# Kernel optimization log

Hardware: AMD Instinct MI355X
Metric: run time of the kernel (lower is better)

## Reference

```python
import jax, jax.numpy as jnp
import numpy as np
from jax import lax

B, N, S, K = 16, 8192, 1024, 32
FACTOR = 1.0
EPS_BN = 1e-5


def farthest_point_sample(xyz, npoint):
    # xyz: [B, N, 3] -> idx [B, npoint]. Deterministic start at index 0
    # (torch version starts at a random index; start choice doesn't change the math pattern).
    b, n, _ = xyz.shape
    bidx = jnp.arange(b)

    def step(carry, _):
        distance, farthest = carry
        centroid = xyz[bidx, farthest]                      # [B, 3]
        dist = jnp.sum((xyz - centroid[:, None, :]) ** 2, -1)  # [B, N]
        distance = jnp.minimum(distance, dist)
        new_far = jnp.argmax(distance, axis=-1)
        return (distance, new_far), farthest

    init = (jnp.full((b, n), 1e10, xyz.dtype), jnp.zeros((b,), jnp.int32))
    _, idxs = lax.scan(step, init, None, length=npoint)
    return idxs.T  # [B, npoint]


def square_distance(src, dst):
    # [B,Ns,3] x [B,Nd,3] -> [B,Ns,Nd]
    d = -2.0 * jnp.einsum('bnc,bmc->bnm', src, dst)
    d += jnp.sum(src ** 2, -1)[:, :, None]
    d += jnp.sum(dst ** 2, -1)[:, None, :]
    return d


def safe_cdist(x):
    # x: [B, C, S]; pairwise euclidean over rows -> [B, C, C]; zero-safe sqrt
    diff = x[:, :, None, :] - x[:, None, :, :]          # [B, C, C, S]
    sq = jnp.sum(diff * diff, -1)
    pos = sq > 0
    return jnp.where(pos, jnp.sqrt(jnp.where(pos, sq, 1.0)), 0.0)


def batchnorm(x, gamma, beta, axes):
    mean = jnp.mean(x, axes, keepdims=True)
    var = jnp.var(x, axes, keepdims=True)  # biased, as in torch BN normalization
    return (x - mean) / jnp.sqrt(var + EPS_BN) * gamma + beta


def reference(xyz, bn1_gamma, bn1_beta, bn2_gamma, bn2_beta):
    b = xyz.shape[0]
    # --- FPS sampling ---
    fps_idx = farthest_point_sample(lax.stop_gradient(xyz), S)          # [B,S]
    new_xyz = jnp.take_along_axis(xyz, fps_idx[:, :, None], axis=1)     # [B,S,3]
    # --- kNN grouping ---
    sq = square_distance(lax.stop_gradient(new_xyz), lax.stop_gradient(xyz))  # [B,S,N]
    _, knn_idx = lax.top_k(-sq, K)                                      # [B,S,K] indices
    grouped = jax.vmap(lambda p, i: p[i])(xyz, knn_idx)                 # [B,S,K,3]
    diff = grouped - new_xyz[:, :, None, :]
    std = jnp.std(diff, ddof=1)                                         # scalar, unbiased like torch.std
    knn_norm = diff / (std + 1e-5)
    center = jnp.broadcast_to(new_xyz[:, :, None, :], (b, S, K, 3))
    knn_xyz = jnp.concatenate([knn_norm, center], axis=-1)              # [B,S,K,6]
    # --- Pooling over neighbors ---
    x = jnp.transpose(knn_xyz, (0, 3, 1, 2))                            # [B,6,S,K]
    lc = jnp.max(x, -1) + jnp.mean(x, -1)                               # [B,6,S]
    lc = jax.nn.relu(batchnorm(lc, bn1_gamma[None, :, None], bn1_beta[None, :, None], (0, 2)))
    # --- Consecutive representation (cdist + superdiagonal factor) ---
    tfcw = safe_cdist(lc)                                               # [B,6,6]
    i = jnp.arange(5)
    tfcw = tfcw.at[:, i, i + 1].multiply(FACTOR)
    # --- Pooling2 ---
    feat = tfcw.reshape(b, -1)                                          # [B,36]
    feat = jax.nn.relu(batchnorm(feat, bn2_gamma[None, :], bn2_beta[None, :], (0,)))
    return feat


def setup_inputs() -> dict:
    key = jax.random.key(0)
    k1, = jax.random.split(key, 1)
    return {
        'xyz': jax.random.normal(k1, (B, N, 3), dtype=jnp.float32),
        'bn1_gamma': jnp.ones((6,), jnp.float32),
        'bn1_beta': jnp.zeros((6,), jnp.float32),
        'bn2_gamma': jnp.ones((36,), jnp.float32),
        'bn2_beta': jnp.zeros((36,), jnp.float32),
    }
```

## Files before the change

kernel.cpp:

```cpp
#include <hip/hip_runtime.h>
#include <hip/hip_bf16.h>

constexpr int BB = 16;
constexpr int NN = 8192;
constexpr int SS = 1024;
constexpr int KK = 32;
constexpr int BUFC = 256;

__device__ __forceinline__ float b2f(__hip_bfloat16 h) { return __bfloat162float(h); }

__device__ __forceinline__ unsigned mkey32(float d) {
    unsigned u = __float_as_uint(d);
    return u ^ (0x80000000u | (unsigned)((int)u >> 31));
}

__device__ __forceinline__ unsigned long long dist_key(const float* __restrict__ pb,
                                                       int idx, float qx, float qy,
                                                       float qz, float qq) {
    float px = pb[idx * 3 + 0];
    float py = pb[idx * 3 + 1];
    float pz = pb[idx * 3 + 2];
    float dot = __fadd_rn(__fadd_rn(__fmul_rn(qx, px), __fmul_rn(qy, py)), __fmul_rn(qz, pz));
    float pp  = __fadd_rn(__fadd_rn(__fmul_rn(px, px), __fmul_rn(py, py)), __fmul_rn(pz, pz));
    float d = __fadd_rn(__fadd_rn(__fmul_rn(-2.0f, dot), qq), pp);
    return ((unsigned long long)mkey32(d) << 32) | (unsigned)idx;
}

template <int CTRL, int RMASK>
__device__ __forceinline__ unsigned long long dppmove_u64(unsigned long long v) {
    int lo = (int)(unsigned)v, hi = (int)(unsigned)(v >> 32);
    int nlo = __builtin_amdgcn_update_dpp(lo, lo, CTRL, RMASK, 0xf, false);
    int nhi = __builtin_amdgcn_update_dpp(hi, hi, CTRL, RMASK, 0xf, false);
    return ((unsigned long long)(unsigned)nhi << 32) | (unsigned)nlo;
}

template <int CTRL, int RMASK>
__device__ __forceinline__ double dppmax_f64(double v) {
    double m = __longlong_as_double(
        dppmove_u64<CTRL, RMASK>((unsigned long long)__double_as_longlong(v)));
    return fmax(v, m);
}

__device__ __forceinline__ double wave_max_dpp_f64(double v) {
    v = dppmax_f64<0x121, 0xf>(v);
    v = dppmax_f64<0x122, 0xf>(v);
    v = dppmax_f64<0x124, 0xf>(v);
    v = dppmax_f64<0x128, 0xf>(v);
    v = dppmax_f64<0x142, 0xa>(v);
    v = dppmax_f64<0x143, 0xc>(v);
    return v;
}

__device__ __forceinline__ unsigned long long bitonic64(unsigned long long v, int lane) {
#pragma unroll
    for (int k = 2; k <= 64; k <<= 1) {
#pragma unroll
        for (int j = k >> 1; j > 0; j >>= 1) {
            unsigned long long p = __shfl_xor(v, j);
            bool up = ((lane & k) == 0);
            bool lower = ((lane & j) == 0);
            bool take_min = (up == lower);
            v = take_min ? (p < v ? p : v) : (p > v ? p : v);
        }
    }
    return v;
}

__device__ __forceinline__ unsigned expand3(unsigned v) {
    v &= 0x3FFu;
    v = (v | (v << 16)) & 0x030000FFu;
    v = (v | (v << 8))  & 0x0300F00Fu;
    v = (v | (v << 4))  & 0x030C30C3u;
    v = (v | (v << 2))  & 0x09249249u;
    return v;
}

__global__ __launch_bounds__(256) void convert_kernel(
    const void* __restrict__ xyz_raw, const void* __restrict__ g1r,
    const void* __restrict__ b1r, const void* __restrict__ g2r,
    const void* __restrict__ b2r, float* __restrict__ xyzf,
    float* __restrict__ params, void* __restrict__ out_raw) {
    const unsigned short* u = (const unsigned short*)xyz_raw;
    unsigned short s = u[2 * (threadIdx.x & 63)];
    int e = (s >> 7) & 0xFF;
    unsigned long long m = __ballot(e >= 100 && e <= 140);
    bool isbf = __popcll(m) > 48;

    const int NT = BB * NN * 3;
    int tid = blockIdx.x * blockDim.x + threadIdx.x;
    int stride = gridDim.x * blockDim.x;
    if (isbf) {
        const __hip_bfloat16* p = (const __hip_bfloat16*)xyz_raw;
        for (int i = tid; i < NT; i += stride) xyzf[i] = b2f(p[i]);
    } else {
        const float* p = (const float*)xyz_raw;
        for (int i = tid; i < NT; i += stride) xyzf[i] = p[i];
    }
    if (blockIdx.x == 0 && threadIdx.x < 85) {
        int t = threadIdx.x;
        if (t == 84) {
            params[84] = isbf ? 1.0f : 0.0f;
        } else {
            const void* src; int off;
            if (t < 6)       { src = g1r; off = t; }
            else if (t < 12) { src = b1r; off = t - 6; }
            else if (t < 48) { src = g2r; off = t - 12; }
            else             { src = b2r; off = t - 48; }
            params[t] = isbf ? b2f(((const __hip_bfloat16*)src)[off])
                             : ((const float*)src)[off];
        }
    }
    if (blockIdx.x == 1 && threadIdx.x < 64) {
        for (int i = threadIdx.x; i < 576; i += 64) {
            if (isbf) ((__hip_bfloat16*)out_raw)[i] = __float2bfloat16(1.0f);
            else      ((float*)out_raw)[i] = 1.0f;
        }
    }
}

__global__ __attribute__((amdgpu_flat_work_group_size(512, 512)))
__attribute__((amdgpu_waves_per_eu(2, 2)))
void fps_kernel(const float* __restrict__ xyzf, float* __restrict__ new_xyz) {
    constexpr int T = 512, P = NN / T;
    const int b = blockIdx.x, t = threadIdx.x;
    const float* xb = xyzf + (size_t)b * NN * 3;

    __shared__ float sxyz[NN * 3];
    __shared__ unsigned sortk[NN];
    __shared__ double skey[2][8];
    __shared__ float sred[6][8];
    __shared__ float sbb[6];

    for (int i = t; i < NN * 3; i += T) sxyz[i] = xb[i];
    __syncthreads();

    {
        float mn[3] = {3.4e38f, 3.4e38f, 3.4e38f};
        float mx[3] = {-3.4e38f, -3.4e38f, -3.4e38f};
        for (int j = 0; j < P; j++) {
            int p = t + j * T;
#pragma unroll
            for (int c = 0; c < 3; c++) {
                float v = sxyz[p * 3 + c];
                mn[c] = fminf(mn[c], v);
                mx[c] = fmaxf(mx[c], v);
            }
        }
#pragma unroll
        for (int o = 32; o > 0; o >>= 1) {
#pragma unroll
            for (int c = 0; c < 3; c++) {
                mn[c] = fminf(mn[c], __shfl_xor(mn[c], o));
                mx[c] = fmaxf(mx[c], __shfl_xor(mx[c], o));
            }
        }
        int wv = t >> 6, ln = t & 63;
        if (ln == 0) {
#pragma unroll
            for (int c = 0; c < 3; c++) { sred[c][wv] = mn[c]; sred[3 + c][wv] = mx[c]; }
        }
        __syncthreads();
        if (t < 6) {
            bool ismin = t < 3;
            float v = sred[t][0];
            for (int w = 1; w < 8; w++) v = ismin ? fminf(v, sred[t][w]) : fmaxf(v, sred[t][w]);
            sbb[t] = v;
        }
        __syncthreads();
    }

    {
        float bx = sbb[0], by = sbb[1], bz = sbb[2];
        float qsx = 63.0f / fmaxf(sbb[3] - bx, 1e-9f);
        float qsy = 63.0f / fmaxf(sbb[4] - by, 1e-9f);
        float qsz = 63.0f / fmaxf(sbb[5] - bz, 1e-9f);
        for (int p = t; p < NN; p += T) {
            unsigned qx = (unsigned)min(63, (int)((sxyz[p * 3 + 0] - bx) * qsx));
            unsigned qy = (unsigned)min(63, (int)((sxyz[p * 3 + 1] - by) * qsy));
            unsigned qz = (unsigned)min(63, (int)((sxyz[p * 3 + 2] - bz) * qsz));
            unsigned m = (expand3(qx) << 2) | (expand3(qy) << 1) | expand3(qz);
            sortk[p] = (m << 13) | (unsigned)p;
        }
        __syncthreads();
        for (unsigned k = 2; k <= (unsigned)NN; k <<= 1) {
            for (unsigned j = k >> 1; j > 0; j >>= 1) {
#pragma unroll
                for (int r = 0; r < NN / 2 / T; r++) {
                    unsigned gid = (unsigned)(r * T + t);
                    unsigned i = ((gid & ~(j - 1)) << 1) | (gid & (j - 1));
                    unsigned p2 = i | j;
                    unsigned a = sortk[i], c2 = sortk[p2];
                    bool up = ((i & k) == 0);
                    if ((a > c2) == up) { sortk[i] = c2; sortk[p2] = a; }
                }
                __syncthreads();
            }
        }
    }

    float px[P], py[P], pz[P], ds[P];
    int nidx[P];
    float lox = 3.4e38f, loy = 3.4e38f, loz = 3.4e38f;
    float hix = -3.4e38f, hiy = -3.4e38f, hiz = -3.4e38f;
#pragma unroll
    for (int j = 0; j < P; j++) {
        unsigned oi = sortk[t * P + j] & 8191u;
        float x = sxyz[oi * 3 + 0];
        float y = sxyz[oi * 3 + 1];
        float z = sxyz[oi * 3 + 2];
        px[j] = x; py[j] = y; pz[j] = z;
        ds[j] = 1e10f;
        nidx[j] = (int)~oi;
        lox = fminf(lox, x); hix = fmaxf(hix, x);
        loy = fminf(loy, y); hiy = fmaxf(hiy, y);
        loz = fminf(loz, z); hiz = fmaxf(hiz, z);
    }

    float cx = xb[0], cy = xb[1], cz = xb[2];
    if (t == 0) {
        float* o = new_xyz + (size_t)b * SS * 3;
        o[0] = cx; o[1] = cy; o[2] = cz;
    }
    const int wave = t >> 6, lane = t & 63;

    double bk = 0.0;
    float tb = 1e10f;

    for (int step = 1; step < SS; step++) {
        float ax = fmaxf(fmaxf(__fsub_rn(lox, cx), __fsub_rn(cx, hix)), 0.0f);
        float ay = fmaxf(fmaxf(__fsub_rn(loy, cy), __fsub_rn(cy, hiy)), 0.0f);
        float az = fmaxf(fmaxf(__fsub_rn(loz, cz), __fsub_rn(cz, hiz)), 0.0f);
        float lbd = ax * ax + ay * ay + az * az;
        if (lbd * 0.999f < tb) {
            double nbk = 0.0;
#pragma unroll
            for (int j = 0; j < P; j++) {
                float dx = __fsub_rn(px[j], cx);
                float dy = __fsub_rn(py[j], cy);
                float dz = __fsub_rn(pz[j], cz);
                float d = __fadd_rn(__fadd_rn(__fmul_rn(dx, dx), __fmul_rn(dy, dy)),
                                    __fmul_rn(dz, dz));
                float mm = fminf(ds[j], d);
                ds[j] = mm;
                double kk = __hiloint2double(__float_as_int(mm), nidx[j]);
                nbk = fmax(nbk, kk);
            }
            bk = nbk;
            tb = __uint_as_float((unsigned)__double2hiint(bk));
        }

        double wk = wave_max_dpp_f64(bk);
        const int par = step & 1;
        if (lane == 63) skey[par][wave] = wk;
        __syncthreads();

        double k0 = fmax(skey[par][0], skey[par][1]);
        double k1 = fmax(skey[par][2], skey[par][3]);
        double k2 = fmax(skey[par][4], skey[par][5]);
        double k3 = fmax(skey[par][6], skey[par][7]);
        double bkk = fmax(fmax(k0, k1), fmax(k2, k3));

        unsigned gidx = ~(unsigned)(unsigned long long)__double_as_longlong(bkk);
        cx = sxyz[gidx * 3 + 0];
        cy = sxyz[gidx * 3 + 1];
        cz = sxyz[gidx * 3 + 2];
        if (t == 0) {
            float* o = new_xyz + ((size_t)b * SS + step) * 3;
            o[0] = cx; o[1] = cy; o[2] = cz;
        }
    }
}

__global__ __launch_bounds__(256, 2) void knn_kernel(const float* __restrict__ xyzf,
                                                     const float* __restrict__ new_xyz,
                                                     float* __restrict__ A,
                                                     double* __restrict__ qstats) {
    __shared__ unsigned long long buf[4][BUFC];
    const int t = threadIdx.x;
    const int lane = t & 63, wv = t >> 6;
    const int w = blockIdx.x * 4 + wv;
    const int b = w >> 10, s = w & 1023;

    const float* q = new_xyz + ((size_t)b * SS + s) * 3;
    float qx = q[0], qy = q[1], qz = q[2];
    float qq = __fadd_rn(__fadd_rn(__fmul_rn(qx, qx), __fmul_rn(qy, qy)), __fmul_rn(qz, qz));

    const float* pb = xyzf + (size_t)b * NN * 3;
    const unsigned long long ltmask = (1ull << lane) - 1ull;

    unsigned long long lmin = ~0ull;
    for (int j = 0; j < 128; j++) {
        unsigned long long key = dist_key(pb, j * 64 + lane, qx, qy, qz, qq);
        lmin = key < lmin ? key : lmin;
    }

    unsigned long long vs = bitonic64(lmin, lane);
    unsigned long long That = __shfl(vs, 31);

    for (int i = lane; i < BUFC; i += 64) buf[wv][i] = ~0ull;
    int base = 0;
    for (int j = 0; j < 128; j++) {
        unsigned long long key = dist_key(pb, j * 64 + lane, qx, qy, qz, qq);
        bool f = key <= That;
        unsigned long long bal = __ballot(f);
        int pos = base + __popcll(bal & ltmask);
        if (f && pos < BUFC) buf[wv][pos] = key;
        base += __popcll(bal);
    }

    if (base > BUFC) {
        unsigned lo = 0, hi = (unsigned)(That >> 32);
        for (int it = 0; it < 32; it++) {
            unsigned mid = lo + ((hi - lo) >> 1);
            int c = 0;
            for (int j = 0; j < 128; j++) {
                unsigned long long key = dist_key(pb, j * 64 + lane, qx, qy, qz, qq);
                c += ((unsigned)(key >> 32) <= mid) ? 1 : 0;
            }
#pragma unroll
            for (int o = 32; o > 0; o >>= 1) c += __shfl_xor(c, o);
            if (c >= 32) hi = mid; else lo = mid + 1;
        }
        That = ((unsigned long long)hi << 32) | 0xFFFFFFFFull;
        for (int i = lane; i < BUFC; i += 64) buf[wv][i] = ~0ull;
        base = 0;
        for (int j = 0; j < 128; j++) {
            unsigned long long key = dist_key(pb, j * 64 + lane, qx, qy, qz, qq);
            bool f = key <= That;
            unsigned long long bal = __ballot(f);
            int pos = base + __popcll(bal & ltmask);
            if (f && pos < BUFC) buf[wv][pos] = key;
            base += __popcll(bal);
        }
        if (base > BUFC) base = BUFC;
    }

    int M = base;
    unsigned long long kept = ~0ull;
    if (M <= 64) {
        unsigned long long v = (lane < M) ? buf[wv][lane] : ~0ull;
        v = bitonic64(v, lane);
        kept = v;
    } else {
        unsigned long long c0 = buf[wv][lane];
        unsigned long long c1 = buf[wv][64 + lane];
        unsigned long long c2 = buf[wv][128 + lane];
        unsigned long long c3 = buf[wv][192 + lane];
        for (int r = 0; r < KK; r++) {
            unsigned long long m01 = c0 < c1 ? c0 : c1;
            unsigned long long m23 = c2 < c3 ? c2 : c3;
            unsigned long long mm = m01 < m23 ? m01 : m23;
#pragma unroll
            for (int o = 32; o > 0; o >>= 1) {
                unsigned long long t2 = __shfl_xor(mm, o);
                mm = t2 < mm ? t2 : mm;
            }
            if (lane == r) kept = mm;
            c0 = (c0 == mm) ? ~0ull : c0;
            c1 = (c1 == mm) ? ~0ull : c1;
            c2 = (c2 == mm) ? ~0ull : c2;
            c3 = (c3 == mm) ? ~0ull : c3;
        }
    }

    bool act = (lane < KK);
    float gx = 0.0f, gy = 0.0f, gz = 0.0f;
    if (act) {
        unsigned nidx = (unsigned)kept;
        gx = pb[nidx * 3 + 0];
        gy = pb[nidx * 3 + 1];
        gz = pb[nidx * 3 + 2];
    }
    float dx = __fsub_rn(gx, qx);
    float dy = __fsub_rn(gy, qy);
    float dz = __fsub_rn(gz, qz);
    float mx = act ? dx : -3.402823466e38f;
    float my = act ? dy : -3.402823466e38f;
    float mz = act ? dz : -3.402823466e38f;
    float sx = act ? dx : 0.0f;
    float sy = act ? dy : 0.0f;
    float sz = act ? dz : 0.0f;
    double s1 = act ? ((double)dx + (double)dy + (double)dz) : 0.0;
    double s2 = act ? ((double)dx * dx + (double)dy * dy + (double)dz * dz) : 0.0;
#pragma unroll
    for (int o = 32; o > 0; o >>= 1) {
        mx = fmaxf(mx, __shfl_xor(mx, o));
        my = fmaxf(my, __shfl_xor(my, o));
        mz = fmaxf(mz, __shfl_xor(mz, o));
        sx += __shfl_xor(sx, o);
        sy += __shfl_xor(sy, o);
        sz += __shfl_xor(sz, o);
        s1 += __shfl_xor(s1, o);
        s2 += __shfl_xor(s2, o);
    }
    if (lane == 0) {
        float* a = A + ((size_t)b * SS + s) * 3;
        a[0] = __fadd_rn(mx, __fmul_rn(sx, 0.03125f));
        a[1] = __fadd_rn(my, __fmul_rn(sy, 0.03125f));
        a[2] = __fadd_rn(mz, __fmul_rn(sz, 0.03125f));
        qstats[2 * w + 0] = s1;
        qstats[2 * w + 1] = s2;
    }
}

__global__ __launch_bounds__(256) void reduce_stats_kernel(const double* __restrict__ qstats,
                                                           double* __restrict__ stats) {
    __shared__ double r1[4], r2[4];
    int t = threadIdx.x;
    double a = 0.0, bsum = 0.0;
    for (int i = t; i < BB * SS; i += 256) { a += qstats[2 * i]; bsum += qstats[2 * i + 1]; }
#pragma unroll
    for (int o = 32; o > 0; o >>= 1) { a += __shfl_xor(a, o); bsum += __shfl_xor(bsum, o); }
    int wv = t >> 6, ln = t & 63;
    if (ln == 0) { r1[wv] = a; r2[wv] = bsum; }
    __syncthreads();
    if (t == 0) {
        stats[0] = r1[0] + r1[1] + r1[2] + r1[3];
        stats[1] = r2[0] + r2[1] + r2[2] + r2[3];
    }
}

__global__ __launch_bounds__(256) void lc_kernel(const float* __restrict__ new_xyz,
                                                 const float* __restrict__ A,
                                                 const double* __restrict__ stats,
                                                 float* __restrict__ lc,
                                                 double* __restrict__ bn1acc) {
    __shared__ double red[4];
    const int b = blockIdx.x / 6, c = blockIdx.x % 6;
    const int t = threadIdx.x;
    const double n = (double)BB * SS * KK * 3;
    double sd = stats[0], sq = stats[1];
    double var = (sq - sd * sd / n) / (n - 1.0);
    float stdv = (float)sqrt(var);
    float denom = __fadd_rn(stdv, 1e-5f);

    double s1 = 0.0, s2 = 0.0;
    for (int r = 0; r < 4; r++) {
        int s = r * 256 + t;
        float v;
        if (c < 3) {
            v = A[((size_t)b * SS + s) * 3 + c] / denom;
        } else {
            float ww = new_xyz[((size_t)b * SS + s) * 3 + (c - 3)];
            v = __fadd_rn(ww, ww);
        }
        lc[((size_t)b * 6 + c) * SS + s] = v;
        s1 += (double)v;
        s2 += (double)v * (double)v;
    }
#pragma unroll
    for (int off = 32; off > 0; off >>= 1) { s1 += __shfl_down(s1, off); s2 += __shfl_down(s2, off); }
    int wv = t >> 6, ln = t & 63;
    if (ln == 0) red[wv] = s1;
    __syncthreads();
    if (t == 0) atomicAdd(&bn1acc[c * 2 + 0], red[0] + red[1] + red[2] + red[3]);
    __syncthreads();
    if (ln == 0) red[wv] = s2;
    __syncthreads();
    if (t == 0) atomicAdd(&bn1acc[c * 2 + 1], red[0] + red[1] + red[2] + red[3]);
}

__global__ __launch_bounds__(256) void cdist_kernel(const float* __restrict__ lc,
                                                    const double* __restrict__ bn1acc,
                                                    const float* __restrict__ params,
                                                    float* __restrict__ tf) {
    __shared__ float sy[6 * SS];
    const int b = blockIdx.x, t = threadIdx.x;
    float mean[6], sde[6], gg[6], bt[6];
    const double n = (double)BB * SS;
#pragma unroll
    for (int c = 0; c < 6; c++) {
        double m = bn1acc[c * 2 + 0] / n;
        double v = bn1acc[c * 2 + 1] / n - m * m;
        mean[c] = (float)m;
        sde[c] = sqrtf((float)v + 1e-5f);
        gg[c] = params[c];
        bt[c] = params[6 + c];
    }
    for (int r = 0; r < 24; r++) {
        int g = r * 256 + t;
        int c = g >> 10;
        float v = lc[(size_t)b * 6 * SS + g];
        float y = (v - mean[c]) / sde[c] * gg[c] + bt[c];
        sy[g] = fmaxf(y, 0.0f);
    }
    __syncthreads();
    if (t < 6) tf[b * 36 + t * 7] = 0.0f;

    const int w = t >> 6, lane = t & 63;
    const int PI[15] = {0,0,0,0,0,1,1,1,1,2,2,2,3,3,4};
    const int PJ[15] = {1,2,3,4,5,2,3,4,5,3,4,5,4,5,5};
    for (int r = 0; r < 4; r++) {
        int p = w + r * 4;
        if (p < 15) {
            int i = PI[p], j = PJ[p];
            float acc = 0.0f;
            for (int m2 = 0; m2 < 16; m2++) {
                int s = lane + m2 * 64;
                float d = sy[i * SS + s] - sy[j * SS + s];
                acc += d * d;
            }
#pragma unroll
            for (int off = 32; off > 0; off >>= 1) acc += __shfl_down(acc, off);
            if (lane == 0) {
                float v = acc > 0.0f ? sqrtf(acc) : 0.0f;
                const float FACTOR = 1.0f;
                tf[b * 36 + i * 6 + j] = (j == i + 1) ? v * FACTOR : v;
                tf[b * 36 + j * 6 + i] = v;
            }
        }
    }
}

__global__ __launch_bounds__(64) void bn2_kernel(const float* __restrict__ tf,
                                                 const float* __restrict__ params,
                                                 void* __restrict__ out_raw) {
    int f = threadIdx.x;
    if (f >= 36) return;
    bool isbf = params[84] != 0.0f;
    float x[16]; float sum = 0.0f;
#pragma unroll
    for (int b = 0; b < 16; b++) { x[b] = tf[b * 36 + f]; sum += x[b]; }
    float mean = sum * 0.0625f;
    float vs = 0.0f;
#pragma unroll
    for (int b = 0; b < 16; b++) { float d = x[b] - mean; vs += d * d; }
    float var = vs * 0.0625f;
    float denom = sqrtf(var + 1e-5f);
    float g = params[12 + f], bb = params[48 + f];
#pragma unroll
    for (int b = 0; b < 16; b++) {
        float y = (x[b] - mean) / denom * g + bb;
        y = fmaxf(y, 0.0f);
        if (isbf) ((__hip_bfloat16*)out_raw)[b * 36 + f] = __float2bfloat16(y);
        else      ((float*)out_raw)[b * 36 + f] = y;
    }
}

extern "C" void kernel_launch(void* const* d_in, const int* in_sizes, int n_in,
                              void* d_out, int out_size, void* d_ws, size_t ws_size,
                              hipStream_t stream) {
    const void* xyz_raw = d_in[0];
    const void* g1r = d_in[1]; const void* b1r = d_in[2];
    const void* g2r = d_in[3]; const void* b2r = d_in[4];
    {
        const void* six[2] = {nullptr, nullptr}; int n6 = 0;
        const void* t36[2] = {nullptr, nullptr}; int n36 = 0;
        const void* big = nullptr;
        for (int i = 0; i < n_in; i++) {
            if (in_sizes[i] == BB * NN * 3) big = d_in[i];
            else if (in_sizes[i] == 6  && n6  < 2) six[n6++]  = d_in[i];
            else if (in_sizes[i] == 36 && n36 < 2) t36[n36++] = d_in[i];
        }
        if (big && n6 == 2 && n36 == 2) {
            xyz_raw = big; g1r = six[0]; b1r = six[1]; g2r = t36[0]; b2r = t36[1];
        }
    }

    char* ws = (char*)d_ws;
    float* xyzf    = (float*)(ws + 0);
    float* new_xyz = (float*)(ws + 1572864);
    float* A       = (float*)(ws + 1769472);
    float* lc      = (float*)(ws + 1966080);
    float* tf      = (float*)(ws + 2359296);
    double* stats  = (double*)(ws + 2361600);
    double* bn1acc = stats + 2;
    float* params  = (float*)(ws + 2361712);
    double* qstats = (double*)(ws + 2362112);

    hipMemsetAsync(stats, 0, 14 * sizeof(double), stream);
    hipLaunchKernelGGL(convert_kernel, dim3(512), dim3(256), 0, stream,
                       xyz_raw, g1r, b1r, g2r, b2r, xyzf, params, d_out);
    hipLaunchKernelGGL(fps_kernel,          dim3(16),   dim3(512), 0, stream, xyzf, new_xyz);
    hipLaunchKernelGGL(knn_kernel,          dim3(4096), dim3(256), 0, stream, xyzf, new_xyz, A, qstats);
    hipLaunchKernelGGL(reduce_stats_kernel, dim3(1),    dim3(256), 0, stream, qstats, stats);
    hipLaunchKernelGGL(lc_kernel,           dim3(96),   dim3(256), 0, stream, new_xyz, A, stats, lc, bn1acc);
    hipLaunchKernelGGL(cdist_kernel,        dim3(16),   dim3(256), 0, stream, lc, bn1acc, params, tf);
    hipLaunchKernelGGL(bn2_kernel,          dim3(1),    dim3(64),  0, stream, tf, params, d_out);

    (void)in_sizes; (void)n_in; (void)out_size; (void)ws_size;
}
```

Before: 1.183 ms.

## Split FPS per-thread points into two culled halves and skip idle wave reductions

Each thread's 16 points are split into two halves, each with its own bounding box and cached max, so the distance update can be skipped for one half when its box lower bound cannot beat the half's current maximum. The wave-level max reduction runs only when some lane in the wave actually updated; otherwise the previous wave max is reused. The winning lane publishes its coordinates next to its key in shared memory, removing the dependent shared-memory lookup of the centroid after the barrier. This adds branches and registers, and relies on the matching lane to write the key, so ties or stale wave values must stay consistent.

```diff
diff --git a/kernel.cpp b/kernel.cpp
--- a/kernel.cpp
+++ b/kernel.cpp
@@ -73,6 +73,15 @@
     v = (v | (v << 4))  & 0x030C30C3u;
     v = (v | (v << 2))  & 0x09249249u;
     return v;
+}
+
+__device__ __forceinline__ void sel2(double& k, float& x, float& y, float& z,
+                                     double kb, float xb, float yb, float zb) {
+    bool g = kb > k;
+    k = g ? kb : k;
+    x = g ? xb : x;
+    y = g ? yb : y;
+    z = g ? zb : z;
 }
 
 __global__ __launch_bounds__(256) void convert_kernel(
@@ -128,6 +137,7 @@
     __shared__ float sxyz[NN * 3];
     __shared__ unsigned sortk[NN];
     __shared__ double skey[2][8];
+    __shared__ float4 scoord[2][8];
     __shared__ float sred[6][8];
     __shared__ float sbb[6];
 
@@ -200,8 +210,10 @@
 
     float px[P], py[P], pz[P], ds[P];
     int nidx[P];
-    float lox = 3.4e38f, loy = 3.4e38f, loz = 3.4e38f;
-    float hix = -3.4e38f, hiy = -3.4e38f, hiz = -3.4e38f;
+    float l0x = 3.4e38f, l0y = 3.4e38f, l0z = 3.4e38f;
+    float h0x = -3.4e38f, h0y = -3.4e38f, h0z = -3.4e38f;
+    float l1x = 3.4e38f, l1y = 3.4e38f, l1z = 3.4e38f;
+    float h1x = -3.4e38f, h1y = -3.4e38f, h1z = -3.4e38f;
 #pragma unroll
     for (int j = 0; j < P; j++) {
         unsigned oi = sortk[t * P + j] & 8191u;
@@ -211,10 +223,18 @@
         px[j] = x; py[j] = y; pz[j] = z;
         ds[j] = 1e10f;
         nidx[j] = (int)~oi;
-        lox = fminf(lox, x); hix = fmaxf(hix, x);
-        loy = fminf(loy, y); hiy = fmaxf(hiy, y);
-        loz = fminf(loz, z); hiz = fmaxf(hiz, z);
-    }
+        if (j < 8) {
+            l0x = fminf(l0x, x); h0x = fmaxf(h0x, x);
+            l0y = fminf(l0y, y); h0y = fmaxf(h0y, y);
+            l0z = fminf(l0z, z); h0z = fmaxf(h0z, z);
+        } else {
+            l1x = fminf(l1x, x); h1x = fmaxf(h1x, x);
+            l1y = fminf(l1y, y); h1y = fmaxf(h1y, y);
+            l1z = fminf(l1z, z); h1z = fmaxf(h1z, z);
+        }
+    }
+    const float lox = fminf(l0x, l1x), loy = fminf(l0y, l1y), loz = fminf(l0z, l1z);
+    const float hix = fmaxf(h0x, h1x), hiy = fmaxf(h0y, h1y), hiz = fmaxf(h0z, h1z);
 
     float cx = xb[0], cy = xb[1], cz = xb[2];
     if (t == 0) {
@@ -223,47 +243,98 @@
     }
     const int wave = t >> 6, lane = t & 63;
 
-    double bk = 0.0;
-    float tb = 1e10f;
+    double hk0 = 0.0, hk1 = 0.0;
+    float tb0 = 1e10f, tb1 = 1e10f;
+    unsigned wkL = 0u, wkH = 0u;
 
     for (int step = 1; step < SS; step++) {
-        float ax = fmaxf(fmaxf(__fsub_rn(lox, cx), __fsub_rn(cx, hix)), 0.0f);
-        float ay = fmaxf(fmaxf(__fsub_rn(loy, cy), __fsub_rn(cy, hiy)), 0.0f);
-        float az = fmaxf(fmaxf(__fsub_rn(loz, cz), __fsub_rn(cz, hiz)), 0.0f);
-        float lbd = ax * ax + ay * ay + az * az;
-        if (lbd * 0.999f < tb) {
-            double nbk = 0.0;
-#pragma unroll
-            for (int j = 0; j < P; j++) {
-                float dx = __fsub_rn(px[j], cx);
-                float dy = __fsub_rn(py[j], cy);
-                float dz = __fsub_rn(pz[j], cz);
-                float d = __fadd_rn(__fadd_rn(__fmul_rn(dx, dx), __fmul_rn(dy, dy)),
-                                    __fmul_rn(dz, dz));
-                float mm = fminf(ds[j], d);
-                ds[j] = mm;
-                double kk = __hiloint2double(__float_as_int(mm), nidx[j]);
-                nbk = fmax(nbk, kk);
-            }
-            bk = nbk;
-            tb = __uint_as_float((unsigned)__double2hiint(bk));
-        }
-
-        double wk = wave_max_dpp_f64(bk);
+        float ax = fmaxf(fmaxf(lox - cx, cx - hix), 0.0f);
+        float ay = fmaxf(fmaxf(loy - cy, cy - hiy), 0.0f);
+        float az = fmaxf(fmaxf(loz - cz, cz - hiz), 0.0f);
+        float lbdO = ax * ax + ay * ay + az * az;
+        bool did = false;
+        if (lbdO * 0.999f < fmaxf(tb0, tb1)) {
+            float a0x = fmaxf(fmaxf(l0x - cx, cx - h0x), 0.0f);
+            float a0y = fmaxf(fmaxf(l0y - cy, cy - h0y), 0.0f);
+            float a0z = fmaxf(fmaxf(l0z - cz, cz - h0z), 0.0f);
+            float lbd0 = a0x * a0x + a0y * a0y + a0z * a0z;
+            if (lbd0 * 0.999f < tb0) {
+                double kk[8];
+#pragma unroll
+                for (int j = 0; j < 8; j++) {
+                    float dx = __fsub_rn(px[j], cx);
+                    float dy = __fsub_rn(py[j], cy);
+                    float dz = __fsub_rn(pz[j], cz);
+                    float d = __fadd_rn(__fadd_rn(__fmul_rn(dx, dx), __fmul_rn(dy, dy)),
+                                        __fmul_rn(dz, dz));
+                    float mm = fminf(ds[j], d);
+                    ds[j] = mm;
+                    kk[j] = __hiloint2double(__float_as_int(mm), nidx[j]);
+                }
+                double m0 = fmax(kk[0], kk[1]), m1 = fmax(kk[2], kk[3]);
+                double m2 = fmax(kk[4], kk[5]), m3 = fmax(kk[6], kk[7]);
+                hk0 = fmax(fmax(m0, m1), fmax(m2, m3));
+                tb0 = __uint_as_float((unsigned)__double2hiint(hk0));
+                did = true;
+            }
+            float a1x = fmaxf(fmaxf(l1x - cx, cx - h1x), 0.0f);
+            float a1y = fmaxf(fmaxf(l1y - cy, cy - h1y), 0.0f);
+            float a1z = fmaxf(fmaxf(l1z - cz, cz - h1z), 0.0f);
+            float lbd1 = a1x * a1x + a1y * a1y + a1z * a1z;
+            if (lbd1 * 0.999f < tb1) {
+                double kk[8];
+#pragma unroll
+                for (int j = 0; j < 8; j++) {
+                    float dx = __fsub_rn(px[8 + j], cx);
+                    float dy = __fsub_rn(py[8 + j], cy);
+                    float dz = __fsub_rn(pz[8 + j], cz);
+                    float d = __fadd_rn(__fadd_rn(__fmul_rn(dx, dx), __fmul_rn(dy, dy)),
+                                        __fmul_rn(dz, dz));
+                    float mm = fminf(ds[8 + j], d);
+                    ds[8 + j] = mm;
+                    kk[j] = __hiloint2double(__float_as_int(mm), nidx[8 + j]);
+                }
+                double m0 = fmax(kk[0], kk[1]), m1 = fmax(kk[2], kk[3]);
+                double m2 = fmax(kk[4], kk[5]), m3 = fmax(kk[6], kk[7]);
+                hk1 = fmax(fmax(m0, m1), fmax(m2, m3));
+                tb1 = __uint_as_float((unsigned)__double2hiint(hk1));
+                did = true;
+            }
+        }
+        double bk = fmax(hk0, hk1);
+        unsigned long long bkb = (unsigned long long)__double_as_longlong(bk);
+
+        unsigned myi = ~(unsigned)bkb;
+        float gx = sxyz[myi * 3 + 0];
+        float gy = sxyz[myi * 3 + 1];
+        float gz = sxyz[myi * 3 + 2];
+
+        if (__ballot(did) != 0ull) {
+            double wkv = wave_max_dpp_f64(bk);
+            unsigned long long wb = (unsigned long long)__double_as_longlong(wkv);
+            wkL = (unsigned)__builtin_amdgcn_readlane((int)(unsigned)wb, 63);
+            wkH = (unsigned)__builtin_amdgcn_readlane((int)(unsigned)(wb >> 32), 63);
+        }
+        unsigned long long wkb = ((unsigned long long)wkH << 32) | wkL;
         const int par = step & 1;
-        if (lane == 63) skey[par][wave] = wk;
+        if (bkb == wkb) {
+            skey[par][wave] = bk;
+            scoord[par][wave] = make_float4(gx, gy, gz, 0.0f);
+        }
         __syncthreads();
 
-        double k0 = fmax(skey[par][0], skey[par][1]);
-        double k1 = fmax(skey[par][2], skey[par][3]);
-        double k2 = fmax(skey[par][4], skey[par][5]);
-        double k3 = fmax(skey[par][6], skey[par][7]);
-        double bkk = fmax(fmax(k0, k1), fmax(k2, k3));
-
-        unsigned gidx = ~(unsigned)(unsigned long long)__double_as_longlong(bkk);
-        cx = sxyz[gidx * 3 + 0];
-        cy = sxyz[gidx * 3 + 1];
-        cz = sxyz[gidx * 3 + 2];
+        double K0 = skey[par][0], K1 = skey[par][1], K2 = skey[par][2], K3 = skey[par][3];
+        double K4 = skey[par][4], K5 = skey[par][5], K6 = skey[par][6], K7 = skey[par][7];
+        float4 C0 = scoord[par][0], C1 = scoord[par][1], C2 = scoord[par][2], C3 = scoord[par][3];
+        float4 C4 = scoord[par][4], C5 = scoord[par][5], C6 = scoord[par][6], C7 = scoord[par][7];
+        sel2(K0, C0.x, C0.y, C0.z, K1, C1.x, C1.y, C1.z);
+        sel2(K2, C2.x, C2.y, C2.z, K3, C3.x, C3.y, C3.z);
+        sel2(K4, C4.x, C4.y, C4.z, K5, C5.x, C5.y, C5.z);
+        sel2(K6, C6.x, C6.y, C6.z, K7, C7.x, C7.y, C7.z);
+        sel2(K0, C0.x, C0.y, C0.z, K2, C2.x, C2.y, C2.z);
+        sel2(K4, C4.x, C4.y, C4.z, K6, C6.x, C6.y, C6.z);
+        sel2(K0, C0.x, C0.y, C0.z, K4, C4.x, C4.y, C4.z);
+        cx = C0.x; cy = C0.y; cz = C0.z;
         if (t == 0) {
             float* o = new_xyz + ((size_t)b * SS + step) * 3;
             o[0] = cx; o[1] = cy; o[2] = cz;
```

New measurement: 1.686 ms. 1.42x slower.
